# Optimization experiments

Hardware: AMD Instinct MI355X
Metric: run time of the kernel (lower is better)

## Reference

```python
import jax, jax.numpy as jnp
import numpy as np

BETA = 0.9
THR = 1.0
ALPHA = 2.0  # snntorch surrogate.atan default

@jax.custom_vjp
def atan_spike(x):
    return (x > 0).astype(x.dtype)

def _atan_fwd(x):
    return atan_spike(x), x

def _atan_bwd(x, g):
    # snntorch ATan surrogate: alpha/2 / (1 + (pi/2 * alpha * x)^2)
    return (g * (ALPHA / 2.0) / (1.0 + (jnp.pi / 2.0 * ALPHA * x) ** 2),)

atan_spike.defvjp(_atan_fwd, _atan_bwd)

def setup_inputs() -> dict:
    key = jax.random.key(0)
    k = jax.random.split(key, 5)
    B, T, C, H, W = 128, 25, 3, 64, 64
    F, HID, O = C * H * W, 2048, 2
    bound1 = 1.0 / np.sqrt(F)
    boundo = 1.0 / np.sqrt(HID)
    return {
        "x": jax.random.normal(k[0], (B, T, C, H, W), jnp.float32),
        "W1": jax.random.uniform(k[1], (HID, F), jnp.float32, -bound1, bound1),
        "b1": jax.random.uniform(k[2], (HID,), jnp.float32, -bound1, bound1),
        "Wo": jax.random.uniform(k[3], (O, HID), jnp.float32, -boundo, boundo),
        "bo": jax.random.uniform(k[4], (O,), jnp.float32, -boundo, boundo),
    }

def reference(x, W1, b1, Wo, bo):
    B, T = x.shape[0], x.shape[1]
    HID, O = W1.shape[0], Wo.shape[0]
    xf = x.reshape(B, T, -1).transpose(1, 0, 2)  # [T, B, F]
    # fc1 for all timesteps at once (input is fixed per step)
    h_all = jnp.einsum('tbf,hf->tbh', xf, W1) + b1  # [T, B, HID]

    def step(carry, h):
        mem1, memo = carry
        # snntorch Leaky (reset_mechanism='subtract'): reset from previous mem
        r1 = atan_spike(mem1 - THR)
        mem1 = BETA * mem1 + h - r1 * THR
        s1 = atan_spike(mem1 - THR)
        o = s1 @ Wo.T + bo
        ro = atan_spike(memo - THR)
        memo = BETA * memo + o - ro * THR
        so = atan_spike(memo - THR)
        return (mem1, memo), so

    init = (jnp.zeros((B, HID), x.dtype), jnp.zeros((B, O), x.dtype))
    (_, _), spk_rec = jax.lax.scan(step, init, h_all)
    # train=False path: sum of output spikes over time
    return spk_rec.sum(axis=0)  # [B, O]
```

## Files before the change

kernel.cpp:

```cpp
#include <hip/hip_runtime.h>


#define T_STEPS 25
#define B_SZ    128
#define F_SZ    12288
#define HID_SZ  2048
#define KT      384
#define A_CH    32768
#define B_CH    16384
#define M_PAD   3328

typedef __attribute__((ext_vector_type(8))) _Float16 f16x8;
typedef __attribute__((ext_vector_type(4))) float f32x4;

__device__ __forceinline__ void g2l16(const void* g, void* l) {
  __builtin_amdgcn_global_load_lds(
      (const __attribute__((address_space(1))) void*)g,
      (__attribute__((address_space(3))) void*)l, 16, 0, 0);
}

__global__ __launch_bounds__(256) void conv_x_kernel(
    const float* __restrict__ x, char* __restrict__ A2) {
  const int total = 13 * KT * 256 * 4;
  for (int i = blockIdx.x * 256 + threadIdx.x; i < total; i += gridDim.x * 256) {
    const int s = i & 3;
    const int r = (i >> 2) & 255;
    const int rest = i >> 10;
    const int ks = rest % KT;
    const int mt = rest / KT;
    const int m = mt * 256 + r;
    const int b = m & 127;
    const int t = m >> 7;
    f16x8 hi = {0, 0, 0, 0, 0, 0, 0, 0};
    f16x8 lo = {0, 0, 0, 0, 0, 0, 0, 0};
    if (t < T_STEPS) {
      const float* src = x + ((size_t)(b * T_STEPS + t)) * F_SZ + ks * 32 + s * 8;
      float4 v0 = *(const float4*)src;
      float4 v1 = *(const float4*)(src + 4);
      float vf[8] = {v0.x, v0.y, v0.z, v0.w, v1.x, v1.y, v1.z, v1.w};
#pragma unroll
      for (int j = 0; j < 8; ++j) {
        _Float16 h = (_Float16)vf[j];
        hi[j] = h;
        lo[j] = (_Float16)(vf[j] - (float)h);
      }
    }
    char* chunk = A2 + (size_t)rest * A_CH;
    *(f16x8*)(chunk + s * 4096 + r * 16) = hi;
    *(f16x8*)(chunk + (s + 4) * 4096 + r * 16) = lo;
  }
}

__global__ __launch_bounds__(256) void conv_w_kernel(
    const float* __restrict__ W1, char* __restrict__ B2) {
  const int total = 16 * KT * 128 * 4;
  for (int i = blockIdx.x * 256 + threadIdx.x; i < total; i += gridDim.x * 256) {
    const int s = i & 3;
    const int r = (i >> 2) & 127;
    const int rest = i >> 9;
    const int ks = rest % KT;
    const int nt = rest / KT;
    const float* src = W1 + ((size_t)(nt * 128 + r)) * F_SZ + ks * 32 + s * 8;
    float4 v0 = *(const float4*)src;
    float4 v1 = *(const float4*)(src + 4);
    float vf[8] = {v0.x, v0.y, v0.z, v0.w, v1.x, v1.y, v1.z, v1.w};
    f16x8 hi, lo;
#pragma unroll
    for (int j = 0; j < 8; ++j) {
      float vs = vf[j] * 128.0f;
      _Float16 h = (_Float16)vs;
      hi[j] = h;
      lo[j] = (_Float16)(vs - (float)h);
    }
    char* chunk = B2 + (size_t)rest * B_CH;
    *(f16x8*)(chunk + s * 2048 + r * 16) = hi;
    *(f16x8*)(chunk + (s + 4) * 2048 + r * 16) = lo;
  }
}

__global__ __launch_bounds__(512) void gemm_mfma_kernel(
    const char* __restrict__ A2, const char* __restrict__ B2,
    const float* __restrict__ b1, float* __restrict__ h_all) {
  __shared__ __align__(16) char lds[131072];
  const int tid = threadIdx.x;
  const int l = tid & 63;
  const int w = tid >> 6;
  const int wm = w >> 1;
  const int wn = w & 1;

  const int bid = blockIdx.x;
  const int swz = (bid & 7) * 26 + (bid >> 3);
  const int mt = swz >> 4;
  const int nt = swz & 15;
  const char* aSrc = A2 + (size_t)mt * KT * A_CH;
  const char* bSrc = B2 + (size_t)nt * KT * B_CH;

#define STAGE_A_PAIR(ktx, i0)                                              \
  do {                                                                     \
    const char* s_ = aSrc + (size_t)(ktx) * A_CH + (i0) * 8192 + tid * 16; \
    char* d_ = (char*)lds + ((ktx) % 3) * 32768 + (i0) * 8192 + w * 1024;  \
    g2l16(s_, d_);                                                         \
    g2l16(s_ + 8192, d_ + 8192);                                           \
  } while (0)
#define STAGE_B2(ktx)                                                      \
  do {                                                                     \
    const char* s_ = bSrc + (size_t)(ktx) * B_CH + tid * 16;               \
    char* d_ = (char*)lds + 98304 + ((ktx) & 1) * 16384 + w * 1024;        \
    g2l16(s_, d_);                                                         \
    g2l16(s_ + 8192, d_ + 8192);                                           \
  } while (0)

  f32x4 acc[4][4];
#pragma unroll
  for (int i = 0; i < 4; ++i)
#pragma unroll
    for (int j = 0; j < 4; ++j) acc[i][j] = (f32x4){0.f, 0.f, 0.f, 0.f};

  const int aoff = (l >> 4) * 4096 + (wm * 64 + (l & 15)) * 16;
  const int boff = (l >> 4) * 2048 + (wn * 64 + (l & 15)) * 16;

  STAGE_A_PAIR(0, 0); STAGE_A_PAIR(0, 2); STAGE_B2(0);
  STAGE_A_PAIR(1, 0); STAGE_A_PAIR(1, 2); STAGE_B2(1);

#define MM3(mf, nf, AH, AL, BH, BL)                                                      \
  acc[mf][nf] = __builtin_amdgcn_mfma_f32_16x16x32_f16(AH, BH, acc[mf][nf], 0, 0, 0);    \
  acc[mf][nf] = __builtin_amdgcn_mfma_f32_16x16x32_f16(AH, BL, acc[mf][nf], 0, 0, 0);    \
  acc[mf][nf] = __builtin_amdgcn_mfma_f32_16x16x32_f16(AL, BH, acc[mf][nf], 0, 0, 0);

  for (int kt = 0; kt < KT; ++kt) {
    if (kt == 0) {
      asm volatile("s_waitcnt vmcnt(6)" ::: "memory");
    } else if (kt < KT - 1) {
      asm volatile("s_waitcnt vmcnt(4)" ::: "memory");
    } else {
      asm volatile("s_waitcnt vmcnt(0)" ::: "memory");
    }
    __builtin_amdgcn_s_barrier();
    asm volatile("" ::: "memory");
    __builtin_amdgcn_sched_barrier(0);

    const char* la = (const char*)lds + (kt % 3) * 32768;
    const char* lb = (const char*)lds + 98304 + (kt & 1) * 16384;

    f16x8 ah0 = *(const f16x8*)(la + aoff);
    f16x8 ah1 = *(const f16x8*)(la + aoff + 256);
    f16x8 ah2 = *(const f16x8*)(la + aoff + 512);
    f16x8 ah3 = *(const f16x8*)(la + aoff + 768);
    f16x8 al0 = *(const f16x8*)(la + aoff + 16384);
    f16x8 al1 = *(const f16x8*)(la + aoff + 16384 + 256);
    f16x8 al2 = *(const f16x8*)(la + aoff + 16384 + 512);
    f16x8 al3 = *(const f16x8*)(la + aoff + 16384 + 768);
    f16x8 bh0 = *(const f16x8*)(lb + boff);
    f16x8 bl0 = *(const f16x8*)(lb + boff + 8192);
    f16x8 bh1 = *(const f16x8*)(lb + boff + 256);
    f16x8 bl1 = *(const f16x8*)(lb + boff + 8192 + 256);

    if (kt >= 1 && kt <= KT - 2) STAGE_B2(kt + 1);
    if (kt <= KT - 3) STAGE_A_PAIR(kt + 2, 0);

    __builtin_amdgcn_s_setprio(1);
    MM3(0, 0, ah0, al0, bh0, bl0)
    MM3(1, 0, ah1, al1, bh0, bl0)
    MM3(2, 0, ah2, al2, bh0, bl0)
    MM3(3, 0, ah3, al3, bh0, bl0)
    MM3(0, 1, ah0, al0, bh1, bl1)
    MM3(1, 1, ah1, al1, bh1, bl1)
    MM3(2, 1, ah2, al2, bh1, bl1)
    MM3(3, 1, ah3, al3, bh1, bl1)
    __builtin_amdgcn_s_setprio(0);

    __builtin_amdgcn_s_barrier();

    f16x8 bh2 = *(const f16x8*)(lb + boff + 512);
    f16x8 bl2 = *(const f16x8*)(lb + boff + 8192 + 512);
    f16x8 bh3 = *(const f16x8*)(lb + boff + 768);
    f16x8 bl3 = *(const f16x8*)(lb + boff + 8192 + 768);

    if (kt <= KT - 3) STAGE_A_PAIR(kt + 2, 2);

    __builtin_amdgcn_s_setprio(1);
    MM3(0, 2, ah0, al0, bh2, bl2)
    MM3(1, 2, ah1, al1, bh2, bl2)
    MM3(2, 2, ah2, al2, bh2, bl2)
    MM3(3, 2, ah3, al3, bh2, bl2)
    MM3(0, 3, ah0, al0, bh3, bl3)
    MM3(1, 3, ah1, al1, bh3, bl3)
    MM3(2, 3, ah2, al2, bh3, bl3)
    MM3(3, 3, ah3, al3, bh3, bl3)
    __builtin_amdgcn_s_setprio(0);
  }

  const int row0 = mt * 256 + wm * 64 + (l >> 4) * 4;
  const int col0 = nt * 128 + wn * 64 + (l & 15);
#pragma unroll
  for (int nf = 0; nf < 4; ++nf) {
    const int col = col0 + nf * 16;
    const float bias = b1[col];
#pragma unroll
    for (int mf = 0; mf < 4; ++mf) {
#pragma unroll
      for (int q = 0; q < 4; ++q) {
        const int row = row0 + mf * 16 + q;
        h_all[(size_t)row * HID_SZ + col] = acc[mf][nf][q] * 0.0078125f + bias;
      }
    }
  }
#undef STAGE_A_PAIR
#undef STAGE_B2
#undef MM3
}

__global__ __launch_bounds__(256) void gemm_h_kernel(
    const float* __restrict__ x, const float* __restrict__ W1,
    const float* __restrict__ b1, float* __restrict__ h_all) {
  __shared__ float As[16][128];
  __shared__ float Bs[16][128];
  const int tid = threadIdx.x;
  const int tx = tid & 15;
  const int ty = tid >> 4;
  const int m0 = blockIdx.x * 128;
  const int n0 = blockIdx.y * 128;
  const int lrow = tid >> 1;
  const int lcol = (tid & 1) * 8;
  const int gm = m0 + lrow;
  const int bb = gm & (B_SZ - 1);
  const int tt = gm >> 7;
  const float* aptr = x + ((size_t)bb * T_STEPS + tt) * F_SZ + lcol;
  const float* bptr = W1 + (size_t)(n0 + lrow) * F_SZ + lcol;
  float acc[8][8];
#pragma unroll
  for (int i = 0; i < 8; ++i)
#pragma unroll
    for (int j = 0; j < 8; ++j) acc[i][j] = 0.f;
  for (int k0 = 0; k0 < F_SZ; k0 += 16) {
    float4 av0 = *(const float4*)(aptr + k0);
    float4 av1 = *(const float4*)(aptr + k0 + 4);
    float4 bv0 = *(const float4*)(bptr + k0);
    float4 bv1 = *(const float4*)(bptr + k0 + 4);
    As[lcol + 0][lrow] = av0.x; As[lcol + 1][lrow] = av0.y;
    As[lcol + 2][lrow] = av0.z; As[lcol + 3][lrow] = av0.w;
    As[lcol + 4][lrow] = av1.x; As[lcol + 5][lrow] = av1.y;
    As[lcol + 6][lrow] = av1.z; As[lcol + 7][lrow] = av1.w;
    Bs[lcol + 0][lrow] = bv0.x; Bs[lcol + 1][lrow] = bv0.y;
    Bs[lcol + 2][lrow] = bv0.z; Bs[lcol + 3][lrow] = bv0.w;
    Bs[lcol + 4][lrow] = bv1.x; Bs[lcol + 5][lrow] = bv1.y;
    Bs[lcol + 6][lrow] = bv1.z; Bs[lcol + 7][lrow] = bv1.w;
    __syncthreads();
#pragma unroll
    for (int k = 0; k < 16; ++k) {
      float4 a0 = *(const float4*)&As[k][ty * 8];
      float4 a1 = *(const float4*)&As[k][ty * 8 + 4];
      float4 q0 = *(const float4*)&Bs[k][tx * 8];
      float4 q1 = *(const float4*)&Bs[k][tx * 8 + 4];
      float ar[8] = {a0.x, a0.y, a0.z, a0.w, a1.x, a1.y, a1.z, a1.w};
      float br[8] = {q0.x, q0.y, q0.z, q0.w, q1.x, q1.y, q1.z, q1.w};
#pragma unroll
      for (int i = 0; i < 8; ++i)
#pragma unroll
        for (int j = 0; j < 8; ++j)
          acc[i][j] = fmaf(ar[i], br[j], acc[i][j]);
    }
    __syncthreads();
  }
#pragma unroll
  for (int i = 0; i < 8; ++i) {
    const int gm2 = m0 + ty * 8 + i;
    float* orow = h_all + (size_t)gm2 * HID_SZ + n0 + tx * 8;
    const float* brow = b1 + n0 + tx * 8;
#pragma unroll
    for (int j = 0; j < 8; ++j) orow[j] = acc[i][j] + brow[j];
  }
}

__global__ __launch_bounds__(256) void lif_scan_kernel(
    const float* __restrict__ h_all, const float* __restrict__ Wo,
    const float* __restrict__ bo, float* __restrict__ out) {
  const int b = blockIdx.x;
  const int tid = threadIdx.x;
  float mem1[8];
  float wo0[8], wo1[8];
#pragma unroll
  for (int i = 0; i < 8; ++i) {
    mem1[i] = 0.f;
    wo0[i] = Wo[tid + 256 * i];
    wo1[i] = Wo[HID_SZ + tid + 256 * i];
  }
  __shared__ float partial[4][2];
  float memo0 = 0.f, memo1 = 0.f, acc0 = 0.f, acc1 = 0.f;
  const float bo0 = bo[0], bo1 = bo[1];
  for (int t = 0; t < T_STEPS; ++t) {
    const float* hrow = h_all + ((size_t)t * B_SZ + b) * HID_SZ;
    float p0 = 0.f, p1 = 0.f;
#pragma unroll
    for (int i = 0; i < 8; ++i) {
      float h = hrow[tid + 256 * i];
      float r1 = mem1[i] > 1.0f ? 1.0f : 0.0f;
      float m = 0.9f * mem1[i] + h - r1;
      mem1[i] = m;
      if (m > 1.0f) { p0 += wo0[i]; p1 += wo1[i]; }
    }
#pragma unroll
    for (int off = 32; off > 0; off >>= 1) {
      p0 += __shfl_down(p0, off);
      p1 += __shfl_down(p1, off);
    }
    const int wave = tid >> 6;
    if ((tid & 63) == 0) { partial[wave][0] = p0; partial[wave][1] = p1; }
    __syncthreads();
    if (tid == 0) {
      float o0 = partial[0][0] + partial[1][0] + partial[2][0] + partial[3][0] + bo0;
      float o1 = partial[0][1] + partial[1][1] + partial[2][1] + partial[3][1] + bo1;
      float ro0 = memo0 > 1.0f ? 1.0f : 0.0f;
      float ro1 = memo1 > 1.0f ? 1.0f : 0.0f;
      memo0 = 0.9f * memo0 + o0 - ro0;
      memo1 = 0.9f * memo1 + o1 - ro1;
      acc0 += memo0 > 1.0f ? 1.0f : 0.0f;
      acc1 += memo1 > 1.0f ? 1.0f : 0.0f;
    }
    __syncthreads();
  }
  if (tid == 0) {
    out[b * 2 + 0] = acc0;
    out[b * 2 + 1] = acc1;
  }
}

extern "C" void kernel_launch(void* const* d_in, const int* in_sizes, int n_in,
                              void* d_out, int out_size, void* d_ws, size_t ws_size,
                              hipStream_t stream) {
  const float* x  = (const float*)d_in[0];
  const float* W1 = (const float*)d_in[1];
  const float* b1 = (const float*)d_in[2];
  const float* Wo = (const float*)d_in[3];
  const float* bo = (const float*)d_in[4];
  float* out = (float*)d_out;

  const size_t hall_bytes = (size_t)M_PAD * HID_SZ * 4;
  const size_t a2_bytes = (size_t)13 * KT * A_CH;
  const size_t b2_bytes = (size_t)16 * KT * B_CH;
  char* ws = (char*)d_ws;
  float* h_all = (float*)ws;

  if (ws_size >= hall_bytes + a2_bytes + b2_bytes) {
    char* A2 = ws + hall_bytes;
    char* B2 = A2 + a2_bytes;
    conv_x_kernel<<<2048, 256, 0, stream>>>(x, A2);
    conv_w_kernel<<<2048, 256, 0, stream>>>(W1, B2);
    gemm_mfma_kernel<<<208, 512, 0, stream>>>(A2, B2, b1, h_all);
  } else {
    dim3 grid(25, 16);
    gemm_h_kernel<<<grid, 256, 0, stream>>>(x, W1, b1, h_all);
  }
  lif_scan_kernel<<<B_SZ, 256, 0, stream>>>(h_all, Wo, bo, out);
}
```

Measured before the change: 539.9 us.

## Use 256x256 GEMM tiles with split-K of two and fold reduction into scan

Block tiles grow from 256x128 to 256x256. The reduction dimension is split in two halves, so the grid stays at 208 blocks: 13 M tiles x 8 N tiles x 2 K halves. Each block writes raw partial sums to one of two buffers, and the LIF scan kernel adds them, applies the scale and adds the bias. This doubles MFMA work per LDS byte loaded, but it uses 128 accumulator registers per lane, a simpler double-buffered pipeline with __syncthreads, and doubles the global write and read traffic for h_all.

```diff
diff --git a/kernel.cpp b/kernel.cpp
--- a/kernel.cpp
+++ b/kernel.cpp
@@ -6,8 +6,9 @@
 #define F_SZ    12288
 #define HID_SZ  2048
 #define KT      384
+#define KT2     192
 #define A_CH    32768
-#define B_CH    16384
+#define B_CH    32768
 #define M_PAD   3328
 
 typedef __attribute__((ext_vector_type(8))) _Float16 f16x8;
@@ -53,14 +54,14 @@
 
 __global__ __launch_bounds__(256) void conv_w_kernel(
     const float* __restrict__ W1, char* __restrict__ B2) {
-  const int total = 16 * KT * 128 * 4;
+  const int total = 8 * KT * 256 * 4;
   for (int i = blockIdx.x * 256 + threadIdx.x; i < total; i += gridDim.x * 256) {
     const int s = i & 3;
-    const int r = (i >> 2) & 127;
-    const int rest = i >> 9;
+    const int r = (i >> 2) & 255;
+    const int rest = i >> 10;
     const int ks = rest % KT;
     const int nt = rest / KT;
-    const float* src = W1 + ((size_t)(nt * 128 + r)) * F_SZ + ks * 32 + s * 8;
+    const float* src = W1 + ((size_t)(nt * 256 + r)) * F_SZ + ks * 32 + s * 8;
     float4 v0 = *(const float4*)src;
     float4 v1 = *(const float4*)(src + 4);
     float vf[8] = {v0.x, v0.y, v0.z, v0.w, v1.x, v1.y, v1.z, v1.w};
@@ -73,140 +74,103 @@
       lo[j] = (_Float16)(vs - (float)h);
     }
     char* chunk = B2 + (size_t)rest * B_CH;
-    *(f16x8*)(chunk + s * 2048 + r * 16) = hi;
-    *(f16x8*)(chunk + (s + 4) * 2048 + r * 16) = lo;
-  }
-}
-
-__global__ __launch_bounds__(512) void gemm_mfma_kernel(
+    *(f16x8*)(chunk + s * 4096 + r * 16) = hi;
+    *(f16x8*)(chunk + (s + 4) * 4096 + r * 16) = lo;
+  }
+}
+
+__global__ __launch_bounds__(512, 2) void gemm_mfma_kernel(
     const char* __restrict__ A2, const char* __restrict__ B2,
-    const float* __restrict__ b1, float* __restrict__ h_all) {
+    float* __restrict__ parts) {
   __shared__ __align__(16) char lds[131072];
   const int tid = threadIdx.x;
   const int l = tid & 63;
   const int w = tid >> 6;
-  const int wm = w >> 1;
-  const int wn = w & 1;
+  const int wm = w >> 2;
+  const int wn = w & 3;
 
   const int bid = blockIdx.x;
   const int swz = (bid & 7) * 26 + (bid >> 3);
   const int mt = swz >> 4;
-  const int nt = swz & 15;
-  const char* aSrc = A2 + (size_t)mt * KT * A_CH;
-  const char* bSrc = B2 + (size_t)nt * KT * B_CH;
-
-#define STAGE_A_PAIR(ktx, i0)                                              \
+  const int nt = (swz >> 1) & 7;
+  const int sp = swz & 1;
+  const char* aSrc = A2 + (size_t)(mt * KT + sp * KT2) * A_CH;
+  const char* bSrc = B2 + (size_t)(nt * KT + sp * KT2) * B_CH;
+
+#define STAGE(ktx)                                                         \
   do {                                                                     \
-    const char* s_ = aSrc + (size_t)(ktx) * A_CH + (i0) * 8192 + tid * 16; \
-    char* d_ = (char*)lds + ((ktx) % 3) * 32768 + (i0) * 8192 + w * 1024;  \
-    g2l16(s_, d_);                                                         \
-    g2l16(s_ + 8192, d_ + 8192);                                           \
+    const char* sa_ = aSrc + (size_t)(ktx) * A_CH + tid * 16;              \
+    const char* sb_ = bSrc + (size_t)(ktx) * B_CH + tid * 16;              \
+    char* da_ = (char*)lds + ((ktx) & 1) * 65536 + w * 1024;               \
+    char* db_ = da_ + 32768;                                               \
+    g2l16(sa_, da_);                 g2l16(sa_ + 8192, da_ + 8192);        \
+    g2l16(sa_ + 16384, da_ + 16384); g2l16(sa_ + 24576, da_ + 24576);     \
+    g2l16(sb_, db_);                 g2l16(sb_ + 8192, db_ + 8192);        \
+    g2l16(sb_ + 16384, db_ + 16384); g2l16(sb_ + 24576, db_ + 24576);     \
   } while (0)
-#define STAGE_B2(ktx)                                                      \
-  do {                                                                     \
-    const char* s_ = bSrc + (size_t)(ktx) * B_CH + tid * 16;               \
-    char* d_ = (char*)lds + 98304 + ((ktx) & 1) * 16384 + w * 1024;        \
-    g2l16(s_, d_);                                                         \
-    g2l16(s_ + 8192, d_ + 8192);                                           \
-  } while (0)
-
-  f32x4 acc[4][4];
-#pragma unroll
-  for (int i = 0; i < 4; ++i)
+
+  f32x4 acc[8][4];
+#pragma unroll
+  for (int i = 0; i < 8; ++i)
 #pragma unroll
     for (int j = 0; j < 4; ++j) acc[i][j] = (f32x4){0.f, 0.f, 0.f, 0.f};
 
-  const int aoff = (l >> 4) * 4096 + (wm * 64 + (l & 15)) * 16;
-  const int boff = (l >> 4) * 2048 + (wn * 64 + (l & 15)) * 16;
-
-  STAGE_A_PAIR(0, 0); STAGE_A_PAIR(0, 2); STAGE_B2(0);
-  STAGE_A_PAIR(1, 0); STAGE_A_PAIR(1, 2); STAGE_B2(1);
+  const int aoff = (l >> 4) * 4096 + (wm * 128 + (l & 15)) * 16;
+  const int boff = (l >> 4) * 4096 + (wn * 64 + (l & 15)) * 16;
 
 #define MM3(mf, nf, AH, AL, BH, BL)                                                      \
   acc[mf][nf] = __builtin_amdgcn_mfma_f32_16x16x32_f16(AH, BH, acc[mf][nf], 0, 0, 0);    \
   acc[mf][nf] = __builtin_amdgcn_mfma_f32_16x16x32_f16(AH, BL, acc[mf][nf], 0, 0, 0);    \
   acc[mf][nf] = __builtin_amdgcn_mfma_f32_16x16x32_f16(AL, BH, acc[mf][nf], 0, 0, 0);
 
-  for (int kt = 0; kt < KT; ++kt) {
-    if (kt == 0) {
-      asm volatile("s_waitcnt vmcnt(6)" ::: "memory");
-    } else if (kt < KT - 1) {
-      asm volatile("s_waitcnt vmcnt(4)" ::: "memory");
-    } else {
-      asm volatile("s_waitcnt vmcnt(0)" ::: "memory");
-    }
-    __builtin_amdgcn_s_barrier();
-    asm volatile("" ::: "memory");
-    __builtin_amdgcn_sched_barrier(0);
-
-    const char* la = (const char*)lds + (kt % 3) * 32768;
-    const char* lb = (const char*)lds + 98304 + (kt & 1) * 16384;
-
-    f16x8 ah0 = *(const f16x8*)(la + aoff);
-    f16x8 ah1 = *(const f16x8*)(la + aoff + 256);
-    f16x8 ah2 = *(const f16x8*)(la + aoff + 512);
-    f16x8 ah3 = *(const f16x8*)(la + aoff + 768);
-    f16x8 al0 = *(const f16x8*)(la + aoff + 16384);
-    f16x8 al1 = *(const f16x8*)(la + aoff + 16384 + 256);
-    f16x8 al2 = *(const f16x8*)(la + aoff + 16384 + 512);
-    f16x8 al3 = *(const f16x8*)(la + aoff + 16384 + 768);
-    f16x8 bh0 = *(const f16x8*)(lb + boff);
-    f16x8 bl0 = *(const f16x8*)(lb + boff + 8192);
-    f16x8 bh1 = *(const f16x8*)(lb + boff + 256);
-    f16x8 bl1 = *(const f16x8*)(lb + boff + 8192 + 256);
-
-    if (kt >= 1 && kt <= KT - 2) STAGE_B2(kt + 1);
-    if (kt <= KT - 3) STAGE_A_PAIR(kt + 2, 0);
-
-    __builtin_amdgcn_s_setprio(1);
-    MM3(0, 0, ah0, al0, bh0, bl0)
-    MM3(1, 0, ah1, al1, bh0, bl0)
-    MM3(2, 0, ah2, al2, bh0, bl0)
-    MM3(3, 0, ah3, al3, bh0, bl0)
-    MM3(0, 1, ah0, al0, bh1, bl1)
-    MM3(1, 1, ah1, al1, bh1, bl1)
-    MM3(2, 1, ah2, al2, bh1, bl1)
-    MM3(3, 1, ah3, al3, bh1, bl1)
-    __builtin_amdgcn_s_setprio(0);
-
-    __builtin_amdgcn_s_barrier();
-
-    f16x8 bh2 = *(const f16x8*)(lb + boff + 512);
-    f16x8 bl2 = *(const f16x8*)(lb + boff + 8192 + 512);
-    f16x8 bh3 = *(const f16x8*)(lb + boff + 768);
-    f16x8 bl3 = *(const f16x8*)(lb + boff + 8192 + 768);
-
-    if (kt <= KT - 3) STAGE_A_PAIR(kt + 2, 2);
-
-    __builtin_amdgcn_s_setprio(1);
-    MM3(0, 2, ah0, al0, bh2, bl2)
-    MM3(1, 2, ah1, al1, bh2, bl2)
-    MM3(2, 2, ah2, al2, bh2, bl2)
-    MM3(3, 2, ah3, al3, bh2, bl2)
-    MM3(0, 3, ah0, al0, bh3, bl3)
-    MM3(1, 3, ah1, al1, bh3, bl3)
-    MM3(2, 3, ah2, al2, bh3, bl3)
-    MM3(3, 3, ah3, al3, bh3, bl3)
-    __builtin_amdgcn_s_setprio(0);
-  }
-
-  const int row0 = mt * 256 + wm * 64 + (l >> 4) * 4;
-  const int col0 = nt * 128 + wn * 64 + (l & 15);
+  STAGE(0);
+
+  for (int kt = 0; kt < KT2; ++kt) {
+    __syncthreads();
+    if (kt + 1 < KT2) STAGE(kt + 1);
+
+    const char* la = (const char*)lds + (kt & 1) * 65536;
+    const char* lb = la + 32768;
+
+    f16x8 ah[8], al[8];
+#pragma unroll
+    for (int mf = 0; mf < 8; ++mf) {
+      ah[mf] = *(const f16x8*)(la + aoff + mf * 256);
+      al[mf] = *(const f16x8*)(la + aoff + 16384 + mf * 256);
+    }
+#pragma unroll
+    for (int nf = 0; nf < 4; ++nf) {
+      f16x8 bh = *(const f16x8*)(lb + boff + nf * 256);
+      f16x8 bl = *(const f16x8*)(lb + boff + 16384 + nf * 256);
+      __builtin_amdgcn_s_setprio(1);
+      MM3(0, nf, ah[0], al[0], bh, bl)
+      MM3(1, nf, ah[1], al[1], bh, bl)
+      MM3(2, nf, ah[2], al[2], bh, bl)
+      MM3(3, nf, ah[3], al[3], bh, bl)
+      MM3(4, nf, ah[4], al[4], bh, bl)
+      MM3(5, nf, ah[5], al[5], bh, bl)
+      MM3(6, nf, ah[6], al[6], bh, bl)
+      MM3(7, nf, ah[7], al[7], bh, bl)
+      __builtin_amdgcn_s_setprio(0);
+    }
+  }
+
+  float* dst = parts + (size_t)sp * ((size_t)M_PAD * HID_SZ);
+  const int row0 = mt * 256 + wm * 128 + (l >> 4) * 4;
+  const int col0 = nt * 256 + wn * 64 + (l & 15);
 #pragma unroll
   for (int nf = 0; nf < 4; ++nf) {
     const int col = col0 + nf * 16;
-    const float bias = b1[col];
-#pragma unroll
-    for (int mf = 0; mf < 4; ++mf) {
+#pragma unroll
+    for (int mf = 0; mf < 8; ++mf) {
 #pragma unroll
       for (int q = 0; q < 4; ++q) {
         const int row = row0 + mf * 16 + q;
-        h_all[(size_t)row * HID_SZ + col] = acc[mf][nf][q] * 0.0078125f + bias;
+        dst[(size_t)row * HID_SZ + col] = acc[mf][nf][q];
       }
     }
   }
-#undef STAGE_A_PAIR
-#undef STAGE_B2
+#undef STAGE
 #undef MM3
 }
 
@@ -273,39 +237,47 @@
 }
 
 __global__ __launch_bounds__(256) void lif_scan_kernel(
-    const float* __restrict__ h_all, const float* __restrict__ Wo,
-    const float* __restrict__ bo, float* __restrict__ out) {
+    const float* __restrict__ p0, const float* __restrict__ p1,
+    const float* __restrict__ b1, const float* __restrict__ Wo,
+    const float* __restrict__ bo, float* __restrict__ out, int two_parts) {
   const int b = blockIdx.x;
   const int tid = threadIdx.x;
   float mem1[8];
-  float wo0[8], wo1[8];
+  float wo0[8], wo1[8], bv[8];
 #pragma unroll
   for (int i = 0; i < 8; ++i) {
     mem1[i] = 0.f;
     wo0[i] = Wo[tid + 256 * i];
     wo1[i] = Wo[HID_SZ + tid + 256 * i];
+    bv[i] = b1[tid + 256 * i];
   }
   __shared__ float partial[4][2];
   float memo0 = 0.f, memo1 = 0.f, acc0 = 0.f, acc1 = 0.f;
   const float bo0 = bo[0], bo1 = bo[1];
   for (int t = 0; t < T_STEPS; ++t) {
-    const float* hrow = h_all + ((size_t)t * B_SZ + b) * HID_SZ;
-    float p0 = 0.f, p1 = 0.f;
+    const size_t rowb = ((size_t)t * B_SZ + b) * HID_SZ;
+    float p0v = 0.f, p1v = 0.f;
+    float pr0 = 0.f, pr1 = 0.f;
 #pragma unroll
     for (int i = 0; i < 8; ++i) {
-      float h = hrow[tid + 256 * i];
+      const size_t idx = rowb + tid + 256 * i;
+      float h;
+      if (two_parts)
+        h = (p0[idx] + p1[idx]) * 0.0078125f + bv[i];
+      else
+        h = p0[idx];
       float r1 = mem1[i] > 1.0f ? 1.0f : 0.0f;
       float m = 0.9f * mem1[i] + h - r1;
       mem1[i] = m;
-      if (m > 1.0f) { p0 += wo0[i]; p1 += wo1[i]; }
+      if (m > 1.0f) { pr0 += wo0[i]; pr1 += wo1[i]; }
     }
 #pragma unroll
     for (int off = 32; off > 0; off >>= 1) {
-      p0 += __shfl_down(p0, off);
-      p1 += __shfl_down(p1, off);
+      pr0 += __shfl_down(pr0, off);
+      pr1 += __shfl_down(pr1, off);
     }
     const int wave = tid >> 6;
-    if ((tid & 63) == 0) { partial[wave][0] = p0; partial[wave][1] = p1; }
+    if ((tid & 63) == 0) { partial[wave][0] = pr0; partial[wave][1] = pr1; }
     __syncthreads();
     if (tid == 0) {
       float o0 = partial[0][0] + partial[1][0] + partial[2][0] + partial[3][0] + bo0;
@@ -318,6 +290,7 @@
       acc1 += memo1 > 1.0f ? 1.0f : 0.0f;
     }
     __syncthreads();
+    (void)p0v; (void)p1v;
   }
   if (tid == 0) {
     out[b * 2 + 0] = acc0;
@@ -335,21 +308,24 @@
   const float* bo = (const float*)d_in[4];
   float* out = (float*)d_out;
 
-  const size_t hall_bytes = (size_t)M_PAD * HID_SZ * 4;
+  const size_t part_bytes = (size_t)M_PAD * HID_SZ * 4;
   const size_t a2_bytes = (size_t)13 * KT * A_CH;
-  const size_t b2_bytes = (size_t)16 * KT * B_CH;
+  const size_t b2_bytes = (size_t)8 * KT * B_CH;
   char* ws = (char*)d_ws;
-  float* h_all = (float*)ws;
-
-  if (ws_size >= hall_bytes + a2_bytes + b2_bytes) {
-    char* A2 = ws + hall_bytes;
+  float* parts = (float*)ws;
+
+  if (ws_size >= 2 * part_bytes + a2_bytes + b2_bytes) {
+    char* A2 = ws + 2 * part_bytes;
     char* B2 = A2 + a2_bytes;
     conv_x_kernel<<<2048, 256, 0, stream>>>(x, A2);
     conv_w_kernel<<<2048, 256, 0, stream>>>(W1, B2);
-    gemm_mfma_kernel<<<208, 512, 0, stream>>>(A2, B2, b1, h_all);
+    gemm_mfma_kernel<<<208, 512, 0, stream>>>(A2, B2, parts);
+    lif_scan_kernel<<<B_SZ, 256, 0, stream>>>(
+        parts, parts + (size_t)M_PAD * HID_SZ, b1, Wo, bo, out, 1);
   } else {
     dim3 grid(25, 16);
-    gemm_h_kernel<<<grid, 256, 0, stream>>>(x, W1, b1, h_all);
-  }
-  lif_scan_kernel<<<B_SZ, 256, 0, stream>>>(h_all, Wo, bo, out);
-}
+    gemm_h_kernel<<<grid, 256, 0, stream>>>(x, W1, b1, (float*)ws);
+    lif_scan_kernel<<<B_SZ, 256, 0, stream>>>(
+        (const float*)ws, (const float*)ws, b1, Wo, bo, out, 0);
+  }
+}
```

Result: slower. 555.0 us (+2.8%).
